# Performance work log

Hardware: AMD Instinct MI355X
Metric: run time of the kernel (lower is better)

The kernel has to match this reference:

```python
import jax, jax.numpy as jnp
import numpy as np

D = 1024  # input_dim


def setup_inputs() -> dict:
    key = jax.random.key(0)
    ks = jax.random.split(key, 7)
    s = 1.0 / np.sqrt(D)
    return {
        "x": jax.random.normal(ks[0], (4, 2048, D), dtype=jnp.float32),
        "wq": jax.random.normal(ks[1], (D, D), dtype=jnp.float32) * s,
        "bq": jax.random.normal(ks[2], (D,), dtype=jnp.float32) * s,
        "wk": jax.random.normal(ks[3], (D, D), dtype=jnp.float32) * s,
        "bk": jax.random.normal(ks[4], (D,), dtype=jnp.float32) * s,
        "wv": jax.random.normal(ks[5], (D, D), dtype=jnp.float32) * s,
        "bv": jax.random.normal(ks[6], (D,), dtype=jnp.float32) * s,
    }


def reference(x, wq, bq, wk, bk, wv, bv):
    # torch Linear: y = x @ W^T + b
    q = jnp.einsum('btd,ed->bte', x, wq) + bq  # (B,T,D)
    k = jnp.einsum('btd,ed->bte', x, wk) + bk
    v = jnp.einsum('btd,ed->bte', x, wv) + bv
    scale = 1.0 / jnp.sqrt(jnp.asarray(D, dtype=x.dtype))
    scores = jnp.einsum('btd,bsd->bts', q, k) * scale  # (B,T,T)
    attn = jax.nn.softmax(scores, axis=-1)
    return jnp.einsum('bts,bsd->btd', attn, v)
```

## Files before the change

### kernel.cpp

```cpp
#include <hip/hip_runtime.h>
#include <stdint.h>

#define BB 4
#define TT 2048
#define DD 1024

typedef unsigned short u16;
typedef unsigned int u32;
typedef u16 u16x4 __attribute__((ext_vector_type(4)));
typedef u16 u16x8 __attribute__((ext_vector_type(8)));
typedef float f32x4 __attribute__((ext_vector_type(4)));
typedef short s16x8 __attribute__((ext_vector_type(8)));

__device__ __forceinline__ u16 f2bf(float f) {
  u32 u = __float_as_uint(f);
  return (u16)((u + 0x7fffu + ((u >> 16) & 1u)) >> 16);
}
__device__ __forceinline__ float bf2f(u16 h) {
  return __uint_as_float((u32)h << 16);
}

__device__ __forceinline__ void gload_lds16(const void* g, void* l) {
  __builtin_amdgcn_global_load_lds(
      (const __attribute__((address_space(1))) u32*)g,
      (__attribute__((address_space(3))) u32*)l, 16, 0, 0);
}

__device__ __forceinline__ void swizzle_tiles(int& tileM, int& tileN) {
  const int gN = gridDim.x, gM = gridDim.y;
  const int L = blockIdx.y * gN + blockIdx.x;
  const int xcd = L & 7, j = L >> 3;
  const int Mq = gM >> 2, Nq = gN >> 1;
  tileM = (((xcd >> 1) * Mq) + j / Nq) << 7;
  tileN = (((xcd & 1) * Nq) + j % Nq) << 7;
}

__global__ __launch_bounds__(256) void cast_bf16_kernel(
    const float* __restrict__ in, u16* __restrict__ out, int n8) {
  int i = blockIdx.x * 256 + threadIdx.x;
  if (i >= n8) return;
  const f32x4* p = (const f32x4*)in;
  f32x4 a = p[2 * (size_t)i];
  f32x4 b = p[2 * (size_t)i + 1];
  u16x8 o;
  o[0] = f2bf(a[0]); o[1] = f2bf(a[1]); o[2] = f2bf(a[2]); o[3] = f2bf(a[3]);
  o[4] = f2bf(b[0]); o[5] = f2bf(b[1]); o[6] = f2bf(b[2]); o[7] = f2bf(b[3]);
  *(u16x8*)(out + 8 * (size_t)i) = o;
}

__global__ __launch_bounds__(256) void wcast_kernel(
    const float* __restrict__ wq, const float* __restrict__ wk,
    const float* __restrict__ wv, u16* __restrict__ out) {
  int i = blockIdx.x * 256 + threadIdx.x;
  const int n1 = DD * DD / 8;
  const float* src = i < n1 ? wq : (i < 2 * n1 ? wk : wv);
  int ii = i < n1 ? i : (i < 2 * n1 ? i - n1 : i - 2 * n1);
  const f32x4* p = (const f32x4*)src;
  f32x4 a = p[2 * (size_t)ii];
  f32x4 b = p[2 * (size_t)ii + 1];
  u16x8 o;
  o[0] = f2bf(a[0]); o[1] = f2bf(a[1]); o[2] = f2bf(a[2]); o[3] = f2bf(a[3]);
  o[4] = f2bf(b[0]); o[5] = f2bf(b[1]); o[6] = f2bf(b[2]); o[7] = f2bf(b[3]);
  *(u16x8*)(out + 8 * (size_t)i) = o;
}

__global__ __launch_bounds__(256) void bias_concat_kernel(
    const float* __restrict__ bq, const float* __restrict__ bk,
    const float* __restrict__ bv, float* __restrict__ out) {
  int i = blockIdx.x * 256 + threadIdx.x;
  float v = i < DD ? bq[i] : (i < 2 * DD ? bk[i - DD] : bv[i - 2 * DD]);
  out[i] = v;
}

__device__ __forceinline__ void kloop_bt(
    const u16* __restrict__ A, const u16* __restrict__ B, int lda, int ldb,
    int K, int tileM, int tileN, u16* sA, u16* sB, f32x4 acc[4][4]) {
  const int tid = threadIdx.x;
  const int lane = tid & 63;
  const int wave = tid >> 6;
  const int quad = lane >> 4;
  const int l15 = lane & 15;
  const int wm = (wave >> 1) << 6;
  const int wn = (wave & 1) << 6;

  const u16 *gA[4], *gB[4];
  u16 *lA[4], *lB[4];
#pragma unroll
  for (int j = 0; j < 4; ++j) {
    const int ch = wave * 256 + j * 64 + lane;
    const int r = ch >> 3;
    const int cg = ((ch & 7) ^ (r & 7)) * 8;
    gA[j] = A + (size_t)(tileM + r) * lda + cg;
    gB[j] = B + (size_t)(tileN + r) * ldb + cg;
    lA[j] = sA + wave * 2048 + j * 512;
    lB[j] = sB + wave * 2048 + j * 512;
  }

  const int x0 = (quad ^ (l15 & 7)) * 8;
  int aOff[4], bOff[4];
#pragma unroll
  for (int i = 0; i < 4; ++i) {
    aOff[i] = (wm + i * 16 + l15) * 64 + x0;
    bOff[i] = (wn + i * 16 + l15) * 64 + x0;
  }

  for (int it = 0; it < K; it += 64) {
#pragma unroll
    for (int j = 0; j < 4; ++j) gload_lds16(gA[j], lA[j]);
#pragma unroll
    for (int j = 0; j < 4; ++j) gload_lds16(gB[j], lB[j]);
#pragma unroll
    for (int j = 0; j < 4; ++j) { gA[j] += 64; gB[j] += 64; }
    __syncthreads();

    s16x8 af[4], bf[4];
#pragma unroll
    for (int i = 0; i < 4; ++i) af[i] = *(const s16x8*)(sA + aOff[i]);
#pragma unroll
    for (int i = 0; i < 4; ++i) bf[i] = *(const s16x8*)(sB + bOff[i]);
#pragma unroll
    for (int mi = 0; mi < 4; ++mi)
#pragma unroll
      for (int ni = 0; ni < 4; ++ni)
        acc[mi][ni] = __builtin_amdgcn_mfma_f32_16x16x32_bf16(
            af[mi], bf[ni], acc[mi][ni], 0, 0, 0);

#pragma unroll
    for (int i = 0; i < 4; ++i) af[i] = *(const s16x8*)(sA + (aOff[i] ^ 32));
#pragma unroll
    for (int i = 0; i < 4; ++i) bf[i] = *(const s16x8*)(sB + (bOff[i] ^ 32));
#pragma unroll
    for (int mi = 0; mi < 4; ++mi)
#pragma unroll
      for (int ni = 0; ni < 4; ++ni)
        acc[mi][ni] = __builtin_amdgcn_mfma_f32_16x16x32_bf16(
            af[mi], bf[ni], acc[mi][ni], 0, 0, 0);
    __syncthreads();
  }
}

__global__ __launch_bounds__(256, 2) void gemm_qkv(
    const u16* __restrict__ A, const u16* __restrict__ B,
    u16* __restrict__ qk, u16* __restrict__ vt, const float* __restrict__ bias) {
  __shared__ u16 sA[128 * 64];
  __shared__ u16 sB[128 * 64];
  const int lane = threadIdx.x & 63;
  const int wave = threadIdx.x >> 6;
  const int quad = lane >> 4;
  const int l15 = lane & 15;
  const int wm = (wave >> 1) << 6;
  const int wn = (wave & 1) << 6;
  int tileM, tileN;
  swizzle_tiles(tileM, tileN);

  f32x4 acc[4][4] = {};
  kloop_bt(A, B, DD, DD, DD, tileM, tileN, sA, sB, acc);

  const int rowB = tileM + wm + quad * 4;
  const int colB = tileN + wn + l15;
  if (tileN < 2048) {
    const float scale = (tileN < 1024) ? 0.03125f : 1.0f;
#pragma unroll
    for (int mi = 0; mi < 4; ++mi)
#pragma unroll
      for (int r = 0; r < 4; ++r) {
        u16* crow = qk + (size_t)(rowB + mi * 16 + r) * 2048 + colB;
#pragma unroll
        for (int ni = 0; ni < 4; ++ni)
          crow[ni * 16] = f2bf((acc[mi][ni][r] + bias[colB + ni * 16]) * scale);
      }
  } else {
    const int b = tileM >> 11;
    const int tBase = (rowB & 2047);
    u16* vb = vt + (size_t)b * DD * TT;
#pragma unroll
    for (int mi = 0; mi < 4; ++mi)
#pragma unroll
      for (int ni = 0; ni < 4; ++ni) {
        const int e = colB + ni * 16 - 2048;
        const float bs = bias[colB + ni * 16];
        u16x4 o;
#pragma unroll
        for (int r = 0; r < 4; ++r) o[r] = f2bf(acc[mi][ni][r] + bs);
        *(u16x4*)(vb + (size_t)e * TT + tBase + mi * 16) = o;
      }
  }
}

__global__ __launch_bounds__(256, 2) void gemm_s(
    const u16* __restrict__ qk, u16* __restrict__ sbuf,
    float* __restrict__ part) {
  __shared__ u16 sA[128 * 64];
  __shared__ u16 sB[128 * 64];
  const int lane = threadIdx.x & 63;
  const int wave = threadIdx.x >> 6;
  const int quad = lane >> 4;
  const int l15 = lane & 15;
  const int wm = (wave >> 1) << 6;
  const int wn = (wave & 1) << 6;
  int tileM, tileN;
  swizzle_tiles(tileM, tileN);
  const int z = blockIdx.z;

  const u16* A = qk + (size_t)z * TT * 2048;
  const u16* B = qk + (size_t)z * TT * 2048 + 1024;

  f32x4 acc[4][4] = {};
  kloop_bt(A, B, 2048, 2048, 1024, tileM, tileN, sA, sB, acc);

  const int rowB = tileM + wm + quad * 4;
  const int colB = tileN + wn + l15;
  u16* C = sbuf + (size_t)z * TT * 2048;
  const int nIdx2 = (tileN + wn) >> 6;
  float* prow = part + ((size_t)z * 32 + nIdx2) * TT;
#pragma unroll
  for (int mi = 0; mi < 4; ++mi)
#pragma unroll
    for (int r = 0; r < 4; ++r) {
      const int row = rowB + mi * 16 + r;
      u16* crow = C + (size_t)row * 2048 + colB;
      float s = 0.f;
#pragma unroll
      for (int ni = 0; ni < 4; ++ni) {
        const u16 h = f2bf(__expf(acc[mi][ni][r]));
        crow[ni * 16] = h;
        s += bf2f(h);
      }
#pragma unroll
      for (int m = 1; m <= 8; m <<= 1) s += __shfl_xor(s, m, 64);
      if (l15 == 0) prow[row] = s;
    }
}

__global__ __launch_bounds__(256, 2) void gemm_pv(
    const u16* __restrict__ sbuf, const u16* __restrict__ vt,
    float* __restrict__ out, const float* __restrict__ part) {
  __shared__ u16 sA[128 * 64];
  __shared__ u16 sB[128 * 64];
  __shared__ float rowInv[128];
  const int tid = threadIdx.x;
  const int lane = tid & 63;
  const int wave = tid >> 6;
  const int quad = lane >> 4;
  const int l15 = lane & 15;
  const int wm = (wave >> 1) << 6;
  const int wn = (wave & 1) << 6;
  int tileM, tileN;
  swizzle_tiles(tileM, tileN);
  const int z = blockIdx.z;

  if (tid < 128) {
    const float* pp = part + (size_t)z * 32 * TT + tileM + tid;
    float s = 0.f;
#pragma unroll
    for (int j = 0; j < 32; ++j) s += pp[j * TT];
    rowInv[tid] = 1.0f / s;
  }

  const u16* A = sbuf + (size_t)z * TT * 2048;
  const u16* B = vt + (size_t)z * DD * TT;

  f32x4 acc[4][4] = {};
  kloop_bt(A, B, 2048, TT, TT, tileM, tileN, sA, sB, acc);

  const int rowB = tileM + wm + quad * 4;
  const int colB = tileN + wn + l15;
  float* C = out + (size_t)z * TT * DD;
#pragma unroll
  for (int mi = 0; mi < 4; ++mi)
#pragma unroll
    for (int r = 0; r < 4; ++r) {
      const int lrow = wm + quad * 4 + mi * 16 + r;
      const float inv = rowInv[lrow];
      float* crow = C + (size_t)(rowB + mi * 16 + r) * DD + colB;
#pragma unroll
      for (int ni = 0; ni < 4; ++ni) crow[ni * 16] = acc[mi][ni][r] * inv;
    }
}

extern "C" void kernel_launch(void* const* d_in, const int* in_sizes, int n_in,
                              void* d_out, int out_size, void* d_ws,
                              size_t ws_size, hipStream_t stream) {
  const float* x = (const float*)d_in[0];
  const float* wq = (const float*)d_in[1];
  const float* bq = (const float*)d_in[2];
  const float* wk = (const float*)d_in[3];
  const float* bk = (const float*)d_in[4];
  const float* wv = (const float*)d_in[5];
  const float* bv = (const float*)d_in[6];
  float* out = (float*)d_out;

  const size_t MB = 1024 * 1024;
  if (ws_size < 103 * MB) return;
  char* ws = (char*)d_ws;
  u16* xbf = (u16*)(ws);
  float* part = (float*)(ws);
  u16* wcat = (u16*)(ws + 16 * MB);
  float* bcat = (float*)(ws + 22 * MB);
  u16* qk = (u16*)(ws + 23 * MB);
  u16* vt = (u16*)(ws + 55 * MB);
  u16* sbuf = (u16*)(ws + 71 * MB);

  const dim3 blk(256);

  cast_bf16_kernel<<<BB * TT * DD / 8 / 256, blk, 0, stream>>>(
      x, xbf, BB * TT * DD / 8);
  wcast_kernel<<<3 * DD * DD / 8 / 256, blk, 0, stream>>>(wq, wk, wv, wcat);
  bias_concat_kernel<<<12, blk, 0, stream>>>(bq, bk, bv, bcat);

  gemm_qkv<<<dim3(3 * DD / 128, BB * TT / 128, 1), blk, 0, stream>>>(
      xbf, wcat, qk, vt, bcat);

  gemm_s<<<dim3(TT / 128, TT / 128, BB), blk, 0, stream>>>(qk, sbuf, part);

  gemm_pv<<<dim3(DD / 128, TT / 128, BB), blk, 0, stream>>>(
      sbuf, vt, out, part);
}
```

Measured before the change: 234.3 us.

## Stream B operand straight to registers and double-buffer A tiles in LDS

The GEMM k-loop now loads only the A tile into LDS, using two buffers so the next tile's global-to-LDS load overlaps compute and one barrier per step is dropped. The B operand fragments are read directly from global memory into registers, also double-buffered, which removes the B LDS staging. The three preprocessing kernels are merged into one launch to cut launch overhead. In exchange, direct global reads of B give less coalescing and reuse, and holding two register copies of B raises register pressure.

```diff
diff --git a/kernel.cpp b/kernel.cpp
--- a/kernel.cpp
+++ b/kernel.cpp
@@ -35,46 +35,78 @@
   tileN = (((xcd & 1) * Nq) + j % Nq) << 7;
 }
 
-__global__ __launch_bounds__(256) void cast_bf16_kernel(
-    const float* __restrict__ in, u16* __restrict__ out, int n8) {
-  int i = blockIdx.x * 256 + threadIdx.x;
-  if (i >= n8) return;
-  const f32x4* p = (const f32x4*)in;
-  f32x4 a = p[2 * (size_t)i];
-  f32x4 b = p[2 * (size_t)i + 1];
-  u16x8 o;
-  o[0] = f2bf(a[0]); o[1] = f2bf(a[1]); o[2] = f2bf(a[2]); o[3] = f2bf(a[3]);
-  o[4] = f2bf(b[0]); o[5] = f2bf(b[1]); o[6] = f2bf(b[2]); o[7] = f2bf(b[3]);
-  *(u16x8*)(out + 8 * (size_t)i) = o;
-}
-
-__global__ __launch_bounds__(256) void wcast_kernel(
-    const float* __restrict__ wq, const float* __restrict__ wk,
-    const float* __restrict__ wv, u16* __restrict__ out) {
-  int i = blockIdx.x * 256 + threadIdx.x;
-  const int n1 = DD * DD / 8;
-  const float* src = i < n1 ? wq : (i < 2 * n1 ? wk : wv);
-  int ii = i < n1 ? i : (i < 2 * n1 ? i - n1 : i - 2 * n1);
-  const f32x4* p = (const f32x4*)src;
-  f32x4 a = p[2 * (size_t)ii];
-  f32x4 b = p[2 * (size_t)ii + 1];
-  u16x8 o;
-  o[0] = f2bf(a[0]); o[1] = f2bf(a[1]); o[2] = f2bf(a[2]); o[3] = f2bf(a[3]);
-  o[4] = f2bf(b[0]); o[5] = f2bf(b[1]); o[6] = f2bf(b[2]); o[7] = f2bf(b[3]);
-  *(u16x8*)(out + 8 * (size_t)i) = o;
-}
-
-__global__ __launch_bounds__(256) void bias_concat_kernel(
+__global__ __launch_bounds__(256) void prep_kernel(
+    const float* __restrict__ x, const float* __restrict__ wq,
+    const float* __restrict__ wk, const float* __restrict__ wv,
     const float* __restrict__ bq, const float* __restrict__ bk,
-    const float* __restrict__ bv, float* __restrict__ out) {
-  int i = blockIdx.x * 256 + threadIdx.x;
-  float v = i < DD ? bq[i] : (i < 2 * DD ? bk[i - DD] : bv[i - 2 * DD]);
-  out[i] = v;
-}
-
-__device__ __forceinline__ void kloop_bt(
+    const float* __restrict__ bv, u16* __restrict__ xbf,
+    u16* __restrict__ wcat, float* __restrict__ bcat) {
+  const int bid = blockIdx.x;
+  const int tid = threadIdx.x;
+  if (bid < 4096) {
+    const size_t i = (size_t)bid * 256 + tid;
+    const f32x4* p = (const f32x4*)x;
+    f32x4 a = p[2 * i];
+    f32x4 b = p[2 * i + 1];
+    u16x8 o;
+    o[0] = f2bf(a[0]); o[1] = f2bf(a[1]); o[2] = f2bf(a[2]); o[3] = f2bf(a[3]);
+    o[4] = f2bf(b[0]); o[5] = f2bf(b[1]); o[6] = f2bf(b[2]); o[7] = f2bf(b[3]);
+    *(u16x8*)(xbf + 8 * i) = o;
+  } else if (bid < 5632) {
+    const int i = (bid - 4096) * 256 + tid;
+    const int n1 = DD * DD / 8;
+    const float* src = i < n1 ? wq : (i < 2 * n1 ? wk : wv);
+    const int ii = i < n1 ? i : (i < 2 * n1 ? i - n1 : i - 2 * n1);
+    const f32x4* p = (const f32x4*)src;
+    f32x4 a = p[2 * (size_t)ii];
+    f32x4 b = p[2 * (size_t)ii + 1];
+    u16x8 o;
+    o[0] = f2bf(a[0]); o[1] = f2bf(a[1]); o[2] = f2bf(a[2]); o[3] = f2bf(a[3]);
+    o[4] = f2bf(b[0]); o[5] = f2bf(b[1]); o[6] = f2bf(b[2]); o[7] = f2bf(b[3]);
+    *(u16x8*)(wcat + 8 * (size_t)i) = o;
+  } else {
+    const int i = (bid - 5632) * 256 + tid;
+    if (i < 3 * DD) {
+      float v = i < DD ? bq[i] : (i < 2 * DD ? bk[i - DD] : bv[i - 2 * DD]);
+      bcat[i] = v;
+    }
+  }
+}
+
+#define GSTEP(CUR, NXT, PREF)                                              \
+  {                                                                        \
+    __syncthreads();                                                       \
+    if (PREF) {                                                            \
+      u16* dstb = sA + (NXT) * 8192 + wave * 2048;                         \
+      _Pragma("unroll") for (int j = 0; j < 4; ++j) {                      \
+        gload_lds16(gA[j], dstb + j * 512);                                \
+        gA[j] += 64;                                                       \
+      }                                                                    \
+      _Pragma("unroll") for (int ni = 0; ni < 4; ++ni) {                   \
+        bset[NXT][ni][0] = *(const s16x8*)(Bp + voff[ni]);                 \
+        bset[NXT][ni][1] = *(const s16x8*)(Bp + voff[ni] + 64);            \
+      }                                                                    \
+      Bp += 128;                                                           \
+    }                                                                      \
+    const u16* sAc = sA + (CUR) * 8192;                                    \
+    s16x8 af[4];                                                           \
+    _Pragma("unroll") for (int i = 0; i < 4; ++i)                          \
+        af[i] = *(const s16x8*)(sAc + aOff[i]);                            \
+    _Pragma("unroll") for (int mi = 0; mi < 4; ++mi)                       \
+        _Pragma("unroll") for (int ni = 0; ni < 4; ++ni)                   \
+            acc[mi][ni] = __builtin_amdgcn_mfma_f32_16x16x32_bf16(         \
+                af[mi], bset[CUR][ni][0], acc[mi][ni], 0, 0, 0);           \
+    _Pragma("unroll") for (int i = 0; i < 4; ++i)                          \
+        af[i] = *(const s16x8*)(sAc + (aOff[i] ^ 32));                     \
+    _Pragma("unroll") for (int mi = 0; mi < 4; ++mi)                       \
+        _Pragma("unroll") for (int ni = 0; ni < 4; ++ni)                   \
+            acc[mi][ni] = __builtin_amdgcn_mfma_f32_16x16x32_bf16(         \
+                af[mi], bset[CUR][ni][1], acc[mi][ni], 0, 0, 0);           \
+  }
+
+__device__ __forceinline__ void kloop_stream(
     const u16* __restrict__ A, const u16* __restrict__ B, int lda, int ldb,
-    int K, int tileM, int tileN, u16* sA, u16* sB, f32x4 acc[4][4]) {
+    int K, int tileM, int tileN, u16* sA, f32x4 acc[4][4]) {
   const int tid = threadIdx.x;
   const int lane = tid & 63;
   const int wave = tid >> 6;
@@ -83,67 +115,54 @@
   const int wm = (wave >> 1) << 6;
   const int wn = (wave & 1) << 6;
 
-  const u16 *gA[4], *gB[4];
-  u16 *lA[4], *lB[4];
+  const u16* gA[4];
 #pragma unroll
   for (int j = 0; j < 4; ++j) {
     const int ch = wave * 256 + j * 64 + lane;
     const int r = ch >> 3;
     const int cg = ((ch & 7) ^ (r & 7)) * 8;
     gA[j] = A + (size_t)(tileM + r) * lda + cg;
-    gB[j] = B + (size_t)(tileN + r) * ldb + cg;
-    lA[j] = sA + wave * 2048 + j * 512;
-    lB[j] = sB + wave * 2048 + j * 512;
   }
 
   const int x0 = (quad ^ (l15 & 7)) * 8;
-  int aOff[4], bOff[4];
-#pragma unroll
-  for (int i = 0; i < 4; ++i) {
-    aOff[i] = (wm + i * 16 + l15) * 64 + x0;
-    bOff[i] = (wn + i * 16 + l15) * 64 + x0;
-  }
-
-  for (int it = 0; it < K; it += 64) {
-#pragma unroll
-    for (int j = 0; j < 4; ++j) gload_lds16(gA[j], lA[j]);
-#pragma unroll
-    for (int j = 0; j < 4; ++j) gload_lds16(gB[j], lB[j]);
-#pragma unroll
-    for (int j = 0; j < 4; ++j) { gA[j] += 64; gB[j] += 64; }
-    __syncthreads();
-
-    s16x8 af[4], bf[4];
-#pragma unroll
-    for (int i = 0; i < 4; ++i) af[i] = *(const s16x8*)(sA + aOff[i]);
-#pragma unroll
-    for (int i = 0; i < 4; ++i) bf[i] = *(const s16x8*)(sB + bOff[i]);
-#pragma unroll
-    for (int mi = 0; mi < 4; ++mi)
-#pragma unroll
-      for (int ni = 0; ni < 4; ++ni)
-        acc[mi][ni] = __builtin_amdgcn_mfma_f32_16x16x32_bf16(
-            af[mi], bf[ni], acc[mi][ni], 0, 0, 0);
-
-#pragma unroll
-    for (int i = 0; i < 4; ++i) af[i] = *(const s16x8*)(sA + (aOff[i] ^ 32));
-#pragma unroll
-    for (int i = 0; i < 4; ++i) bf[i] = *(const s16x8*)(sB + (bOff[i] ^ 32));
-#pragma unroll
-    for (int mi = 0; mi < 4; ++mi)
-#pragma unroll
-      for (int ni = 0; ni < 4; ++ni)
-        acc[mi][ni] = __builtin_amdgcn_mfma_f32_16x16x32_bf16(
-            af[mi], bf[ni], acc[mi][ni], 0, 0, 0);
-    __syncthreads();
+  int aOff[4];
+#pragma unroll
+  for (int i = 0; i < 4; ++i) aOff[i] = (wm + i * 16 + l15) * 64 + x0;
+
+  const char* Bp = (const char*)(B + (size_t)(tileN + wn) * ldb);
+  u32 voff[4];
+#pragma unroll
+  for (int ni = 0; ni < 4; ++ni)
+    voff[ni] = (u32)(((ni * 16 + l15) * (size_t)ldb + quad * 8) * 2);
+
+  s16x8 bset[2][4][2];
+
+  {
+    u16* dstb = sA + wave * 2048;
+#pragma unroll
+    for (int j = 0; j < 4; ++j) {
+      gload_lds16(gA[j], dstb + j * 512);
+      gA[j] += 64;
+    }
+#pragma unroll
+    for (int ni = 0; ni < 4; ++ni) {
+      bset[0][ni][0] = *(const s16x8*)(Bp + voff[ni]);
+      bset[0][ni][1] = *(const s16x8*)(Bp + voff[ni] + 64);
+    }
+    Bp += 128;
+  }
+
+  const int nIter = K >> 6;
+  for (int it = 0; it < nIter; it += 2) {
+    GSTEP(0, 1, true);
+    GSTEP(1, 0, it + 2 < nIter);
   }
 }
 
 __global__ __launch_bounds__(256, 2) void gemm_qkv(
     const u16* __restrict__ A, const u16* __restrict__ B,
     u16* __restrict__ qk, u16* __restrict__ vt, const float* __restrict__ bias) {
-  __shared__ u16 sA[128 * 64];
-  __shared__ u16 sB[128 * 64];
+  __shared__ u16 sA[2 * 128 * 64];
   const int lane = threadIdx.x & 63;
   const int wave = threadIdx.x >> 6;
   const int quad = lane >> 4;
@@ -154,7 +173,7 @@
   swizzle_tiles(tileM, tileN);
 
   f32x4 acc[4][4] = {};
-  kloop_bt(A, B, DD, DD, DD, tileM, tileN, sA, sB, acc);
+  kloop_stream(A, B, DD, DD, DD, tileM, tileN, sA, acc);
 
   const int rowB = tileM + wm + quad * 4;
   const int colB = tileN + wn + l15;
@@ -190,8 +209,7 @@
 __global__ __launch_bounds__(256, 2) void gemm_s(
     const u16* __restrict__ qk, u16* __restrict__ sbuf,
     float* __restrict__ part) {
-  __shared__ u16 sA[128 * 64];
-  __shared__ u16 sB[128 * 64];
+  __shared__ u16 sA[2 * 128 * 64];
   const int lane = threadIdx.x & 63;
   const int wave = threadIdx.x >> 6;
   const int quad = lane >> 4;
@@ -206,7 +224,7 @@
   const u16* B = qk + (size_t)z * TT * 2048 + 1024;
 
   f32x4 acc[4][4] = {};
-  kloop_bt(A, B, 2048, 2048, 1024, tileM, tileN, sA, sB, acc);
+  kloop_stream(A, B, 2048, 2048, 1024, tileM, tileN, sA, acc);
 
   const int rowB = tileM + wm + quad * 4;
   const int colB = tileN + wn + l15;
@@ -235,8 +253,7 @@
 __global__ __launch_bounds__(256, 2) void gemm_pv(
     const u16* __restrict__ sbuf, const u16* __restrict__ vt,
     float* __restrict__ out, const float* __restrict__ part) {
-  __shared__ u16 sA[128 * 64];
-  __shared__ u16 sB[128 * 64];
+  __shared__ u16 sA[2 * 128 * 64];
   __shared__ float rowInv[128];
   const int tid = threadIdx.x;
   const int lane = tid & 63;
@@ -261,7 +278,7 @@
   const u16* B = vt + (size_t)z * DD * TT;
 
   f32x4 acc[4][4] = {};
-  kloop_bt(A, B, 2048, TT, TT, tileM, tileN, sA, sB, acc);
+  kloop_stream(A, B, 2048, TT, 2048, tileM, tileN, sA, acc);
 
   const int rowB = tileM + wm + quad * 4;
   const int colB = tileN + wn + l15;
@@ -303,10 +320,8 @@
 
   const dim3 blk(256);
 
-  cast_bf16_kernel<<<BB * TT * DD / 8 / 256, blk, 0, stream>>>(
-      x, xbf, BB * TT * DD / 8);
-  wcast_kernel<<<3 * DD * DD / 8 / 256, blk, 0, stream>>>(wq, wk, wv, wcat);
-  bias_concat_kernel<<<12, blk, 0, stream>>>(bq, bk, bv, bcat);
+  prep_kernel<<<5644, blk, 0, stream>>>(x, wq, wk, wv, bq, bk, bv, xbf, wcat,
+                                        bcat);
 
   gemm_qkv<<<dim3(3 * DD / 128, BB * TT / 128, 1), blk, 0, stream>>>(
       xbf, wcat, qk, vt, bcat);
```

New measurement: 364.4 us. 55.5% more time.
